# Optimization experiments

Measured on AMD Instinct MI355X. Metric: run time of the kernel, lower is better.

The kernel has to match this reference:

```python
import jax, jax.numpy as jnp
from jax import lax
import numpy as np

N = 256          # HiPPO order
DT = 1.0 / 4096  # discretization step ~ 1/L
L = 4096         # sequence length
BATCH = 64


def _legt_transition(n):
    # LegT (translated Legendre) HiPPO transition matrices (continuous-time).
    Q = np.arange(n, dtype=np.float64)
    R = (2.0 * Q + 1.0) ** 0.5
    j, i = np.meshgrid(Q, Q)
    A = R[:, None] * np.where(i < j, (-1.0) ** (i - j), 1.0) * R[None, :]
    B = R[:, None]
    return -A, B


def _bilinear_discretize(A, B, dt):
    # scipy.signal.cont2discrete(..., method='bilinear')
    n = A.shape[0]
    I = np.eye(n)
    M = np.linalg.inv(I - (dt / 2.0) * A)
    Ad = M @ (I + (dt / 2.0) * A)
    Bd = (M @ B) * dt
    return Ad, Bd


def setup_inputs() -> dict:
    key = jax.random.key(0)
    A, B = _legt_transition(N)
    Ad, Bd = _bilinear_discretize(A, B, DT)
    inputs = jax.random.normal(key, (L, BATCH), dtype=jnp.float32)
    return {
        "inputs": inputs,
        "A": jnp.asarray(Ad, dtype=jnp.float32),          # (N, N)
        "B": jnp.asarray(Bd.squeeze(-1), dtype=jnp.float32),  # (N,)
    }


def reference(inputs, A, B):
    # inputs: (L, BATCH) -> output cs: (L, BATCH, N)
    u = inputs[..., None]  # (L, BATCH, 1)
    c0 = jnp.zeros((inputs.shape[1], A.shape[0]), dtype=inputs.dtype)  # (BATCH, N)

    def step(c, f):
        # c = F.linear(c, A) + B * f  ==  c @ A^T + B * f
        c = c @ A.T + B * f
        return c, c

    _, cs = lax.scan(step, c0, u)
    return cs
```

## Files before the change

kernel.cpp:

```cpp
#include <hip/hip_runtime.h>
#include <hip/hip_bf16.h>


#define MATF 65536

typedef __attribute__((ext_vector_type(8))) short short8;
typedef __attribute__((ext_vector_type(4))) float f32x4;

__device__ __forceinline__ unsigned short f2bf(float x) {
  union { __hip_bfloat16 h; unsigned short u; } cv;
  cv.h = __float2bfloat16(x);
  return cv.u;
}
__device__ __forceinline__ float bf2f(unsigned short u) {
  union { unsigned short u; __hip_bfloat16 h; } cv;
  cv.u = u;
  return __bfloat162float(cv.h);
}

__device__ __forceinline__ void load16_lds(const void* gsrc, void* ldst) {
  __builtin_amdgcn_global_load_lds(
      (const __attribute__((address_space(1))) unsigned int*)gsrc,
      (__attribute__((address_space(3))) unsigned int*)ldst,
      16, 0, 0);
}

__global__ __launch_bounds__(256) void gemm_nn_batch(
    const float* __restrict__ X, const float* __restrict__ Ys,
    float* __restrict__ Zs, int count)
{
  int g    = blockIdx.x >> 4;
  int tile = blockIdx.x & 15;
  if (g >= count) return;
  const float* Y = Ys + (size_t)g * MATF;
  float*       Z = Zs + (size_t)g * MATF;
  int tr = (tile >> 2) * 64;
  int tc = (tile & 3) * 64;

  __shared__ float As[64][33];
  __shared__ float Bs[32][65];
  int tid = threadIdx.x;
  int tx = tid & 15, ty = tid >> 4;
  float acc[4][4] = {};

  for (int k0 = 0; k0 < 256; k0 += 32) {
#pragma unroll
    for (int p = 0; p < 2; ++p) {
      int idx = tid + p * 256;
      int r = idx >> 3, c4 = (idx & 7) * 4;
      float4 v = *(const float4*)(X + (size_t)(tr + r) * 256 + k0 + c4);
      As[r][c4 + 0] = v.x; As[r][c4 + 1] = v.y; As[r][c4 + 2] = v.z; As[r][c4 + 3] = v.w;
    }
#pragma unroll
    for (int p = 0; p < 2; ++p) {
      int idx = tid + p * 256;
      int r = idx >> 4, c4 = (idx & 15) * 4;
      float4 v = *(const float4*)(Y + (size_t)(k0 + r) * 256 + tc + c4);
      Bs[r][c4 + 0] = v.x; Bs[r][c4 + 1] = v.y; Bs[r][c4 + 2] = v.z; Bs[r][c4 + 3] = v.w;
    }
    __syncthreads();
#pragma unroll
    for (int kk = 0; kk < 32; ++kk) {
      float a[4], b[4];
#pragma unroll
      for (int u = 0; u < 4; ++u) a[u] = As[ty * 4 + u][kk];
#pragma unroll
      for (int v = 0; v < 4; ++v) b[v] = Bs[kk][tx * 4 + v];
#pragma unroll
      for (int u = 0; u < 4; ++u)
#pragma unroll
        for (int v = 0; v < 4; ++v) acc[u][v] += a[u] * b[v];
    }
    __syncthreads();
  }
#pragma unroll
  for (int u = 0; u < 4; ++u)
#pragma unroll
    for (int v = 0; v < 4; ++v)
      Z[(size_t)(tr + ty * 4 + u) * 256 + tc + tx * 4 + v] = acc[u][v];
}

__global__ __launch_bounds__(256) void pow_first(
    const float* __restrict__ A, float* __restrict__ P)
{
  int bid = blockIdx.x, tid = threadIdx.x;
  if (bid >= 16) {
    int blk = bid - 16;
#pragma unroll
    for (int q = 0; q < 4; ++q) {
      int idx = blk * 1024 + q * 256 + tid;
      *(float4*)(P + (size_t)idx * 4) = *(const float4*)(A + (size_t)idx * 4);
    }
    return;
  }
  int tile = bid;
  int tr = (tile >> 2) * 64;
  int tc = (tile & 3) * 64;
  __shared__ float As[64][33];
  __shared__ float Bs[32][65];
  int tx = tid & 15, ty = tid >> 4;
  float acc[4][4] = {};
  for (int k0 = 0; k0 < 256; k0 += 32) {
#pragma unroll
    for (int p = 0; p < 2; ++p) {
      int idx = tid + p * 256;
      int r = idx >> 3, c4 = (idx & 7) * 4;
      float4 v = *(const float4*)(A + (size_t)(tr + r) * 256 + k0 + c4);
      As[r][c4 + 0] = v.x; As[r][c4 + 1] = v.y; As[r][c4 + 2] = v.z; As[r][c4 + 3] = v.w;
    }
#pragma unroll
    for (int p = 0; p < 2; ++p) {
      int idx = tid + p * 256;
      int r = idx >> 4, c4 = (idx & 15) * 4;
      float4 v = *(const float4*)(A + (size_t)(k0 + r) * 256 + tc + c4);
      Bs[r][c4 + 0] = v.x; Bs[r][c4 + 1] = v.y; Bs[r][c4 + 2] = v.z; Bs[r][c4 + 3] = v.w;
    }
    __syncthreads();
#pragma unroll
    for (int kk = 0; kk < 32; ++kk) {
      float a[4], b[4];
#pragma unroll
      for (int u = 0; u < 4; ++u) a[u] = As[ty * 4 + u][kk];
#pragma unroll
      for (int v = 0; v < 4; ++v) b[v] = Bs[kk][tx * 4 + v];
#pragma unroll
      for (int u = 0; u < 4; ++u)
#pragma unroll
        for (int v = 0; v < 4; ++v) acc[u][v] += a[u] * b[v];
    }
    __syncthreads();
  }
#pragma unroll
  for (int u = 0; u < 4; ++u)
#pragma unroll
    for (int v = 0; v < 4; ++v)
      P[(size_t)MATF + (size_t)(tr + ty * 4 + u) * 256 + tc + tx * 4 + v] = acc[u][v];
}

__global__ __launch_bounds__(256) void kv_kernel(
    const float* __restrict__ P, const float* __restrict__ Bv,
    float* __restrict__ Kv)
{
  int j = blockIdx.x;
  int n = threadIdx.x;
  __shared__ float bs[256];
  bs[n] = Bv[n];
  __syncthreads();
  if (j == 0) { Kv[n] = bs[n]; return; }
  const float* M = P + (size_t)(j - 1) * MATF;
  float acc = 0.f;
  for (int m = 0; m < 256; ++m) acc += M[(size_t)n * 256 + m] * bs[m];
  Kv[(size_t)j * 256 + n] = acc;
}

__global__ __launch_bounds__(256) void e_kernel(
    const float* __restrict__ in, const float* __restrict__ Kv,
    float* __restrict__ e)
{
  int k = blockIdx.x >> 6;
  int b = blockIdx.x & 63;
  int n = threadIdx.x;
  __shared__ float fs[64];
  if (n < 64) fs[n] = in[(size_t)(k * 64 + n) * 64 + b];
  __syncthreads();
  float acc = 0.f;
#pragma unroll
  for (int j = 0; j < 64; ++j) acc += Kv[(size_t)j * 256 + n] * fs[63 - j];
  e[((size_t)k * 256 + n) * 64 + b] = acc;
}

__global__ __launch_bounds__(256) void scan_round(
    const float* __restrict__ win, float* __restrict__ wout,
    const float* __restrict__ M, int d,
    float* __restrict__ MSdst,
    const float* __restrict__ P, const float* __restrict__ Kv,
    unsigned short* __restrict__ Gt, int gt_row0, int gt_off)
{
  __shared__ float As[64][33];
  __shared__ float Bs[32][65];
  int bid = blockIdx.x;
  int tid = threadIdx.x;

  if (bid >= gt_off) {
    int r2 = gt_row0 + (bid - gt_off);
    if (r2 >= 16384) return;
    int i = r2 >> 8, n = r2 & 255;
    unsigned short* dst = Gt + (size_t)r2 * 640;
    for (int c = tid; c < 320; c += 256) {
      float x;
      if (c < 64) x = (c <= i) ? Kv[(size_t)(i - c) * 256 + n] : 0.f;
      else        x = P[(size_t)i * MATF + (size_t)n * 256 + (c - 64)];
      unsigned short hi = f2bf(x);
      float lo = x - bf2f(hi);
      dst[c]       = hi;
      dst[320 + c] = f2bf(lo);
    }
    return;
  }
  if (bid >= 256) {
    int tile = bid - 256;
    int tr = (tile >> 2) * 64;
    int tc = (tile & 3) * 64;
    int tx = tid & 15, ty = tid >> 4;
    float acc[4][4] = {};
    for (int k0 = 0; k0 < 256; k0 += 32) {
#pragma unroll
      for (int p = 0; p < 2; ++p) {
        int idx = tid + p * 256;
        int r = idx >> 3, c4 = (idx & 7) * 4;
        float4 v = *(const float4*)(M + (size_t)(tr + r) * 256 + k0 + c4);
        As[r][c4 + 0] = v.x; As[r][c4 + 1] = v.y; As[r][c4 + 2] = v.z; As[r][c4 + 3] = v.w;
      }
#pragma unroll
      for (int p = 0; p < 2; ++p) {
        int idx = tid + p * 256;
        int r = idx >> 4, c4 = (idx & 15) * 4;
        float4 v = *(const float4*)(M + (size_t)(k0 + r) * 256 + tc + c4);
        Bs[r][c4 + 0] = v.x; Bs[r][c4 + 1] = v.y; Bs[r][c4 + 2] = v.z; Bs[r][c4 + 3] = v.w;
      }
      __syncthreads();
#pragma unroll
      for (int kk = 0; kk < 32; ++kk) {
        float a[4], b[4];
#pragma unroll
        for (int u = 0; u < 4; ++u) a[u] = As[ty * 4 + u][kk];
#pragma unroll
        for (int v = 0; v < 4; ++v) b[v] = Bs[kk][tx * 4 + v];
#pragma unroll
        for (int u = 0; u < 4; ++u)
#pragma unroll
          for (int v = 0; v < 4; ++v) acc[u][v] += a[u] * b[v];
      }
      __syncthreads();
    }
#pragma unroll
    for (int u = 0; u < 4; ++u)
#pragma unroll
      for (int v = 0; v < 4; ++v)
        MSdst[(size_t)(tr + ty * 4 + u) * 256 + tc + tx * 4 + v] = acc[u][v];
    return;
  }

  int k  = bid >> 2;
  int rt = bid & 3;
  const float* src = win  + (size_t)k * 16384;
  float*       dst = wout + (size_t)k * 16384;
  if (k < d) {
#pragma unroll
    for (int p = 0; p < 16; ++p) {
      int idx = rt * 4096 + p * 256 + tid;
      dst[idx] = src[idx];
    }
    return;
  }
  const float* v = win + (size_t)(k - d) * 16384;
  int tx = tid & 15, ty = tid >> 4;
  float acc[4][4] = {};
  for (int k0 = 0; k0 < 256; k0 += 32) {
#pragma unroll
    for (int p = 0; p < 2; ++p) {
      int idx = tid + p * 256;
      int r = idx >> 3, c4 = (idx & 7) * 4;
      float4 t4 = *(const float4*)(M + (size_t)(rt * 64 + r) * 256 + k0 + c4);
      As[r][c4 + 0] = t4.x; As[r][c4 + 1] = t4.y; As[r][c4 + 2] = t4.z; As[r][c4 + 3] = t4.w;
    }
#pragma unroll
    for (int p = 0; p < 2; ++p) {
      int idx = tid + p * 256;
      int r = idx >> 4, c4 = (idx & 15) * 4;
      float4 t4 = *(const float4*)(v + (size_t)(k0 + r) * 64 + c4);
      Bs[r][c4 + 0] = t4.x; Bs[r][c4 + 1] = t4.y; Bs[r][c4 + 2] = t4.z; Bs[r][c4 + 3] = t4.w;
    }
    __syncthreads();
#pragma unroll
    for (int kk = 0; kk < 32; ++kk) {
      float a[4], b[4];
#pragma unroll
      for (int u = 0; u < 4; ++u) a[u] = As[ty * 4 + u][kk];
#pragma unroll
      for (int v2 = 0; v2 < 4; ++v2) b[v2] = Bs[kk][tx * 4 + v2];
#pragma unroll
      for (int u = 0; u < 4; ++u)
#pragma unroll
        for (int v2 = 0; v2 < 4; ++v2) acc[u][v2] += a[u] * b[v2];
    }
    __syncthreads();
  }
#pragma unroll
  for (int u = 0; u < 4; ++u)
#pragma unroll
    for (int v2 = 0; v2 < 4; ++v2) {
      int idx = (rt * 64 + ty * 4 + u) * 64 + tx * 4 + v2;
      dst[idx] = src[idx] + acc[u][v2];
    }
}

__global__ __launch_bounds__(320) void build_ht(
    const float* __restrict__ in, const float* __restrict__ w,
    unsigned short* __restrict__ Ht)
{
  int row = blockIdx.x;
  int k = row >> 6, b = row & 63;
  int j = threadIdx.x;
  float x;
  if (j < 64) x = in[(size_t)(k * 64 + j) * 64 + b];
  else        x = (k > 0) ? w[((size_t)(k - 1) * 256 + (j - 64)) * 64 + b] : 0.f;
  unsigned short hi = f2bf(x);
  float lo = x - bf2f(hi);
  Ht[(size_t)row * 640 + j]       = hi;
  Ht[(size_t)row * 640 + 320 + j] = f2bf(lo);
}

__global__ __launch_bounds__(512) void out_gemm(
    const unsigned short* __restrict__ Ht,
    const unsigned short* __restrict__ Gt,
    float* __restrict__ out)
{
  __shared__ char smem[65536];
  char* Ab = smem;
  char* Bb = smem + 32768;

  int bid = blockIdx.x;
  int swz = (bid & 7) * 128 + (bid >> 3);
  int mt = swz >> 6;
  int nt = swz & 63;
  int mrow0 = mt * 256, nrow0 = nt * 256;

  int tid = threadIdx.x;
  int w = tid >> 6, l = tid & 63;
  int wm = w >> 2, wn = w & 3;

  auto stage = [&](const unsigned short* src, int row0, char* lds, int k0) {
#pragma unroll
    for (int it = 0; it < 4; ++it) {
      int L = it * 8192 + tid * 16;
      int row = L >> 7;
      int p = (L >> 4) & 7;
      int o = p ^ (row & 7);
      int h = o >> 2, q = o & 3;
      const void* g = src + (size_t)(row0 + row) * 640 + h * 320 + k0 + q * 8;
      void* dst = lds + (it * 8192 + w * 1024);
      load16_lds(g, dst);
    }
  };

  stage(Ht, mrow0, Ab, 0);
  stage(Gt, nrow0, Bb, 0);

  f32x4 acc[8][4] = {};
  int rAbase = wm * 128 + (l & 15);
  int rBbase = wn * 64 + (l & 15);
  int qo = l >> 4;

  for (int ks = 0; ks < 10; ++ks) {
    __syncthreads();
    short8 bh[4], bl[4];
#pragma unroll
    for (int nf = 0; nf < 4; ++nf) {
      int r = rBbase + nf * 16;
      int ph = (qo)     ^ (r & 7);
      int pl = (4 + qo) ^ (r & 7);
      bh[nf] = *(const short8*)(Bb + r * 128 + ph * 16);
      bl[nf] = *(const short8*)(Bb + r * 128 + pl * 16);
    }
#pragma unroll
    for (int mf = 0; mf < 8; ++mf) {
      int r = rAbase + mf * 16;
      int ph = (qo)     ^ (r & 7);
      int pl = (4 + qo) ^ (r & 7);
      short8 ah = *(const short8*)(Ab + r * 128 + ph * 16);
      short8 al = *(const short8*)(Ab + r * 128 + pl * 16);
#pragma unroll
      for (int nf = 0; nf < 4; ++nf) {
        acc[mf][nf] = __builtin_amdgcn_mfma_f32_16x16x32_bf16(ah, bh[nf], acc[mf][nf], 0, 0, 0);
        acc[mf][nf] = __builtin_amdgcn_mfma_f32_16x16x32_bf16(ah, bl[nf], acc[mf][nf], 0, 0, 0);
        acc[mf][nf] = __builtin_amdgcn_mfma_f32_16x16x32_bf16(al, bh[nf], acc[mf][nf], 0, 0, 0);
      }
    }
    __syncthreads();
    if (ks < 9) {
      stage(Ht, mrow0, Ab, (ks + 1) * 32);
      stage(Gt, nrow0, Bb, (ks + 1) * 32);
    }
  }

  int Mbase = mrow0 + wm * 128 + (l >> 4) * 4;
  int Nbase = nrow0 + wn * 64 + (l & 15);
#pragma unroll
  for (int mf = 0; mf < 8; ++mf)
#pragma unroll
    for (int nf = 0; nf < 4; ++nf)
#pragma unroll
      for (int r = 0; r < 4; ++r) {
        int Mrow = Mbase + mf * 16 + r;
        int Ncol = Nbase + nf * 16;
        int k = Mrow >> 6, b = Mrow & 63;
        int i = Ncol >> 8, n = Ncol & 255;
        out[((size_t)k * 4096 + (size_t)i * 64 + b) * 256 + n] = acc[mf][nf][r];
      }
}

extern "C" void kernel_launch(void* const* d_in, const int* in_sizes, int n_in,
                              void* d_out, int out_size, void* d_ws, size_t ws_size,
                              hipStream_t stream)
{
  const float* in = (const float*)d_in[0];
  const float* A  = (const float*)d_in[1];
  const float* Bv = (const float*)d_in[2];
  float* out = (float*)d_out;
  float* ws  = (float*)d_ws;

  float* P  = ws;
  float* Kv = P  + (size_t)64 * MATF;
  float* e  = Kv + (size_t)64 * 256;
  float* w2 = e  + (size_t)64 * 16384;
  float* MS = w2 + (size_t)64 * 16384;
  unsigned short* Ht = (unsigned short*)(MS + (size_t)2 * MATF);
  unsigned short* Gt = Ht + (size_t)4096 * 640;

  pow_first<<<dim3(32), dim3(256), 0, stream>>>(A, P);
  for (int m = 2; m <= 32; m <<= 1) {
    gemm_nn_batch<<<dim3(m * 16), dim3(256), 0, stream>>>(
        P + (size_t)(m - 1) * MATF, P, P + (size_t)m * MATF, m);
  }
  kv_kernel<<<dim3(64), dim3(256), 0, stream>>>(P, Bv, Kv);
  e_kernel<<<dim3(4096), dim3(256), 0, stream>>>(in, Kv, e);

  float* bufs[2] = {e, w2};
  for (int r = 0; r < 6; ++r) {
    const float* M = (r == 0) ? (P + (size_t)63 * MATF)
                              : (MS + (size_t)((r - 1) & 1) * MATF);
    float* MSdst = MS + (size_t)(r & 1) * MATF;
    int gt_row0 = r * 2731;
    int gt_cnt  = (r < 5) ? 2731 : (16384 - 5 * 2731);
    int gt_off  = (r < 5) ? 272 : 256;
    int grid    = gt_off + gt_cnt;
    scan_round<<<dim3(grid), dim3(256), 0, stream>>>(
        bufs[r & 1], bufs[(r + 1) & 1], M, 1 << r,
        MSdst, P, Kv, Gt, gt_row0, gt_off);
  }

  build_ht<<<dim3(4096), dim3(320), 0, stream>>>(in, e, Ht);

  out_gemm<<<dim3(1024), dim3(512), 0, stream>>>(Ht, Gt, out);
}
```

Measured before the change: 384.8 us.

## Double-buffer out_gemm LDS staging with split hi/lo substages and prefetch

The out_gemm main loop now splits each K-step into hi and lo substages. Each substage fills half of a 64KB LDS double buffer, and the next substage is prefetched before the current one computes. Explicit vmcnt waits replace the two __syncthreads, and s_setprio is raised around the MFMA blocks. The LDS swizzle is redone for 64-byte rows. Global loads should now overlap with MFMA work, at the cost of more register pressure from holding ah[8] across substages, plus hand-tuned waitcnt logic that could be fragile.

```diff
diff --git a/kernel.cpp b/kernel.cpp
--- a/kernel.cpp
+++ b/kernel.cpp
@@ -317,8 +317,6 @@
     float* __restrict__ out)
 {
   __shared__ char smem[65536];
-  char* Ab = smem;
-  char* Bb = smem + 32768;
 
   int bid = blockIdx.x;
   int swz = (bid & 7) * 128 + (bid >> 3);
@@ -330,58 +328,87 @@
   int w = tid >> 6, l = tid & 63;
   int wm = w >> 2, wn = w & 3;
 
-  auto stage = [&](const unsigned short* src, int row0, char* lds, int k0) {
-#pragma unroll
-    for (int it = 0; it < 4; ++it) {
-      int L = it * 8192 + tid * 16;
-      int row = L >> 7;
-      int p = (L >> 4) & 7;
-      int o = p ^ (row & 7);
-      int h = o >> 2, q = o & 3;
-      const void* g = src + (size_t)(row0 + row) * 640 + h * 320 + k0 + q * 8;
-      void* dst = lds + (it * 8192 + w * 1024);
-      load16_lds(g, dst);
+  auto stage_ss = [&](int ss) {
+    int h = ss & 1, ks = ss >> 1;
+    char* buf = smem + (ss & 1) * 32768;
+#pragma unroll
+    for (int op = 0; op < 2; ++op) {
+      const unsigned short* src = op ? Gt : Ht;
+      int row0 = op ? nrow0 : mrow0;
+      char* lds = buf + op * 16384;
+#pragma unroll
+      for (int it = 0; it < 2; ++it) {
+        int L = it * 8192 + tid * 16;
+        int row = L >> 6;
+        int p = (L >> 4) & 3;
+        int o = p ^ ((row ^ (row >> 2)) & 3);
+        const void* g = src + (size_t)(row0 + row) * 640 + h * 320 + ks * 32 + o * 8;
+        void* dst = lds + (it * 8192 + w * 1024);
+        load16_lds(g, dst);
+      }
     }
   };
 
-  stage(Ht, mrow0, Ab, 0);
-  stage(Gt, nrow0, Bb, 0);
+  stage_ss(0);
 
   f32x4 acc[8][4] = {};
-  int rAbase = wm * 128 + (l & 15);
-  int rBbase = wn * 64 + (l & 15);
+  short8 ah[8], bh[4];
+  int rA = wm * 128 + (l & 15);
+  int rB = wn * 64 + (l & 15);
   int qo = l >> 4;
 
-  for (int ks = 0; ks < 10; ++ks) {
-    __syncthreads();
-    short8 bh[4], bl[4];
-#pragma unroll
-    for (int nf = 0; nf < 4; ++nf) {
-      int r = rBbase + nf * 16;
-      int ph = (qo)     ^ (r & 7);
-      int pl = (4 + qo) ^ (r & 7);
-      bh[nf] = *(const short8*)(Bb + r * 128 + ph * 16);
-      bl[nf] = *(const short8*)(Bb + r * 128 + pl * 16);
-    }
-#pragma unroll
-    for (int mf = 0; mf < 8; ++mf) {
-      int r = rAbase + mf * 16;
-      int ph = (qo)     ^ (r & 7);
-      int pl = (4 + qo) ^ (r & 7);
-      short8 ah = *(const short8*)(Ab + r * 128 + ph * 16);
-      short8 al = *(const short8*)(Ab + r * 128 + pl * 16);
+#pragma unroll
+  for (int ss = 0; ss < 20; ++ss) {
+    if (ss < 19) {
+      stage_ss(ss + 1);
+      asm volatile("s_waitcnt vmcnt(4)" ::: "memory");
+    } else {
+      asm volatile("s_waitcnt vmcnt(0)" ::: "memory");
+    }
+    __builtin_amdgcn_s_barrier();
+    __builtin_amdgcn_sched_barrier(0);
+    char* Ab = smem + (ss & 1) * 32768;
+    char* Bb = Ab + 16384;
+    if ((ss & 1) == 0) {
 #pragma unroll
       for (int nf = 0; nf < 4; ++nf) {
-        acc[mf][nf] = __builtin_amdgcn_mfma_f32_16x16x32_bf16(ah, bh[nf], acc[mf][nf], 0, 0, 0);
-        acc[mf][nf] = __builtin_amdgcn_mfma_f32_16x16x32_bf16(ah, bl[nf], acc[mf][nf], 0, 0, 0);
-        acc[mf][nf] = __builtin_amdgcn_mfma_f32_16x16x32_bf16(al, bh[nf], acc[mf][nf], 0, 0, 0);
-      }
-    }
-    __syncthreads();
-    if (ks < 9) {
-      stage(Ht, mrow0, Ab, (ks + 1) * 32);
-      stage(Gt, nrow0, Bb, (ks + 1) * 32);
-    }
+        int r = rB + nf * 16;
+        bh[nf] = *(const short8*)(Bb + r * 64 + (qo ^ ((r ^ (r >> 2)) & 3)) * 16);
+      }
+#pragma unroll
+      for (int mf = 0; mf < 8; ++mf) {
+        int r = rA + mf * 16;
+        ah[mf] = *(const short8*)(Ab + r * 64 + (qo ^ ((r ^ (r >> 2)) & 3)) * 16);
+      }
+      __builtin_amdgcn_s_setprio(1);
+#pragma unroll
+      for (int mf = 0; mf < 8; ++mf)
+#pragma unroll
+        for (int nf = 0; nf < 4; ++nf)
+          acc[mf][nf] = __builtin_amdgcn_mfma_f32_16x16x32_bf16(ah[mf], bh[nf], acc[mf][nf], 0, 0, 0);
+      __builtin_amdgcn_s_setprio(0);
+    } else {
+      short8 bl[4];
+#pragma unroll
+      for (int nf = 0; nf < 4; ++nf) {
+        int r = rB + nf * 16;
+        bl[nf] = *(const short8*)(Bb + r * 64 + (qo ^ ((r ^ (r >> 2)) & 3)) * 16);
+      }
+      __builtin_amdgcn_s_setprio(1);
+#pragma unroll
+      for (int mf = 0; mf < 8; ++mf) {
+        int r = rA + mf * 16;
+        short8 al = *(const short8*)(Ab + r * 64 + (qo ^ ((r ^ (r >> 2)) & 3)) * 16);
+#pragma unroll
+        for (int nf = 0; nf < 4; ++nf) {
+          acc[mf][nf] = __builtin_amdgcn_mfma_f32_16x16x32_bf16(ah[mf], bl[nf], acc[mf][nf], 0, 0, 0);
+          acc[mf][nf] = __builtin_amdgcn_mfma_f32_16x16x32_bf16(al, bh[nf], acc[mf][nf], 0, 0, 0);
+        }
+      }
+      __builtin_amdgcn_s_setprio(0);
+    }
+    __builtin_amdgcn_sched_barrier(0);
+    __builtin_amdgcn_s_barrier();
   }
 
   int Mbase = mrow0 + wm * 128 + (l >> 4) * 4;
```

New measurement: 390.2 us. About the same (+1.4%).

## Restructure chunk scan into two-level blocked scan with tiny rounds and fused apply

Applied to the files above, without the earlier changes.

Replaces the six-round full Hillis-Steele scan over 64 chunk states with three rounds inside groups of 8, a small three-round scan over the 8 group carries, and one apply kernel that adds the carries using precomputed powers A^(64q). The apply kernel also writes the bf16 hi/lo H operand directly, replacing build_ht, and the Gt/Ht packing is spread across the scan launches. This cuts the amount of full-size scan GEMM work and removes one pass over the state buffer. In exchange it adds more small launches and extra matrix-power GEMMs.

```diff
diff --git a/kernel.cpp b/kernel.cpp
--- a/kernel.cpp
+++ b/kernel.cpp
@@ -6,6 +6,13 @@
 
 typedef __attribute__((ext_vector_type(8))) short short8;
 typedef __attribute__((ext_vector_type(4))) float f32x4;
+
+struct Sq4 {
+  const float* X[4];
+  const float* Y[4];
+  float* Z[4];
+  int n;
+};
 
 __device__ __forceinline__ unsigned short f2bf(float x) {
   union { __hip_bfloat16 h; unsigned short u; } cv;
@@ -25,47 +32,40 @@
       16, 0, 0);
 }
 
-__global__ __launch_bounds__(256) void gemm_nn_batch(
-    const float* __restrict__ X, const float* __restrict__ Ys,
-    float* __restrict__ Zs, int count)
-{
-  int g    = blockIdx.x >> 4;
-  int tile = blockIdx.x & 15;
-  if (g >= count) return;
-  const float* Y = Ys + (size_t)g * MATF;
-  float*       Z = Zs + (size_t)g * MATF;
+__device__ void tile_gemm64(const float* __restrict__ X,
+                            const float* __restrict__ Y,
+                            float* __restrict__ Z, int tile,
+                            float* As, float* Bs, int tid)
+{
   int tr = (tile >> 2) * 64;
   int tc = (tile & 3) * 64;
-
-  __shared__ float As[64][33];
-  __shared__ float Bs[32][65];
-  int tid = threadIdx.x;
   int tx = tid & 15, ty = tid >> 4;
   float acc[4][4] = {};
-
   for (int k0 = 0; k0 < 256; k0 += 32) {
 #pragma unroll
     for (int p = 0; p < 2; ++p) {
       int idx = tid + p * 256;
       int r = idx >> 3, c4 = (idx & 7) * 4;
       float4 v = *(const float4*)(X + (size_t)(tr + r) * 256 + k0 + c4);
-      As[r][c4 + 0] = v.x; As[r][c4 + 1] = v.y; As[r][c4 + 2] = v.z; As[r][c4 + 3] = v.w;
+      As[r * 33 + c4 + 0] = v.x; As[r * 33 + c4 + 1] = v.y;
+      As[r * 33 + c4 + 2] = v.z; As[r * 33 + c4 + 3] = v.w;
     }
 #pragma unroll
     for (int p = 0; p < 2; ++p) {
       int idx = tid + p * 256;
       int r = idx >> 4, c4 = (idx & 15) * 4;
       float4 v = *(const float4*)(Y + (size_t)(k0 + r) * 256 + tc + c4);
-      Bs[r][c4 + 0] = v.x; Bs[r][c4 + 1] = v.y; Bs[r][c4 + 2] = v.z; Bs[r][c4 + 3] = v.w;
+      Bs[r * 65 + c4 + 0] = v.x; Bs[r * 65 + c4 + 1] = v.y;
+      Bs[r * 65 + c4 + 2] = v.z; Bs[r * 65 + c4 + 3] = v.w;
     }
     __syncthreads();
 #pragma unroll
     for (int kk = 0; kk < 32; ++kk) {
       float a[4], b[4];
 #pragma unroll
-      for (int u = 0; u < 4; ++u) a[u] = As[ty * 4 + u][kk];
-#pragma unroll
-      for (int v = 0; v < 4; ++v) b[v] = Bs[kk][tx * 4 + v];
+      for (int u = 0; u < 4; ++u) a[u] = As[(ty * 4 + u) * 33 + kk];
+#pragma unroll
+      for (int v = 0; v < 4; ++v) b[v] = Bs[kk * 65 + tx * 4 + v];
 #pragma unroll
       for (int u = 0; u < 4; ++u)
 #pragma unroll
@@ -78,6 +78,18 @@
 #pragma unroll
     for (int v = 0; v < 4; ++v)
       Z[(size_t)(tr + ty * 4 + u) * 256 + tc + tx * 4 + v] = acc[u][v];
+}
+
+__global__ __launch_bounds__(256) void gemm_nn_batch(
+    const float* __restrict__ X, const float* __restrict__ Ys,
+    float* __restrict__ Zs, int count)
+{
+  __shared__ float As[64 * 33];
+  __shared__ float Bs[32 * 65];
+  int g    = blockIdx.x >> 4;
+  if (g >= count) return;
+  tile_gemm64(X, Ys + (size_t)g * MATF, Zs + (size_t)g * MATF,
+              blockIdx.x & 15, As, Bs, threadIdx.x);
 }
 
 __global__ __launch_bounds__(256) void pow_first(
@@ -93,48 +105,9 @@
     }
     return;
   }
-  int tile = bid;
-  int tr = (tile >> 2) * 64;
-  int tc = (tile & 3) * 64;
-  __shared__ float As[64][33];
-  __shared__ float Bs[32][65];
-  int tx = tid & 15, ty = tid >> 4;
-  float acc[4][4] = {};
-  for (int k0 = 0; k0 < 256; k0 += 32) {
-#pragma unroll
-    for (int p = 0; p < 2; ++p) {
-      int idx = tid + p * 256;
-      int r = idx >> 3, c4 = (idx & 7) * 4;
-      float4 v = *(const float4*)(A + (size_t)(tr + r) * 256 + k0 + c4);
-      As[r][c4 + 0] = v.x; As[r][c4 + 1] = v.y; As[r][c4 + 2] = v.z; As[r][c4 + 3] = v.w;
-    }
-#pragma unroll
-    for (int p = 0; p < 2; ++p) {
-      int idx = tid + p * 256;
-      int r = idx >> 4, c4 = (idx & 15) * 4;
-      float4 v = *(const float4*)(A + (size_t)(k0 + r) * 256 + tc + c4);
-      Bs[r][c4 + 0] = v.x; Bs[r][c4 + 1] = v.y; Bs[r][c4 + 2] = v.z; Bs[r][c4 + 3] = v.w;
-    }
-    __syncthreads();
-#pragma unroll
-    for (int kk = 0; kk < 32; ++kk) {
-      float a[4], b[4];
-#pragma unroll
-      for (int u = 0; u < 4; ++u) a[u] = As[ty * 4 + u][kk];
-#pragma unroll
-      for (int v = 0; v < 4; ++v) b[v] = Bs[kk][tx * 4 + v];
-#pragma unroll
-      for (int u = 0; u < 4; ++u)
-#pragma unroll
-        for (int v = 0; v < 4; ++v) acc[u][v] += a[u] * b[v];
-    }
-    __syncthreads();
-  }
-#pragma unroll
-  for (int u = 0; u < 4; ++u)
-#pragma unroll
-    for (int v = 0; v < 4; ++v)
-      P[(size_t)MATF + (size_t)(tr + ty * 4 + u) * 256 + tc + tx * 4 + v] = acc[u][v];
+  __shared__ float As[64 * 33];
+  __shared__ float Bs[32 * 65];
+  tile_gemm64(A, A, P + MATF, bid, As, Bs, tid);
 }
 
 __global__ __launch_bounds__(256) void kv_kernel(
@@ -169,21 +142,21 @@
   e[((size_t)k * 256 + n) * 64 + b] = acc;
 }
 
-__global__ __launch_bounds__(256) void scan_round(
+__global__ __launch_bounds__(256) void scan_round2(
     const float* __restrict__ win, float* __restrict__ wout,
-    const float* __restrict__ M, int d,
-    float* __restrict__ MSdst,
+    const float* __restrict__ M, int d, Sq4 sq, int fc_cnt,
     const float* __restrict__ P, const float* __restrict__ Kv,
-    unsigned short* __restrict__ Gt, int gt_row0, int gt_off)
-{
-  __shared__ float As[64][33];
-  __shared__ float Bs[32][65];
-  int bid = blockIdx.x;
-  int tid = threadIdx.x;
-
-  if (bid >= gt_off) {
-    int r2 = gt_row0 + (bid - gt_off);
-    if (r2 >= 16384) return;
+    const float* __restrict__ in, unsigned short* __restrict__ Gt,
+    unsigned short* __restrict__ Ht, int gt_row0)
+{
+  __shared__ float As[64 * 33];
+  __shared__ float Bs[32 * 65];
+  int bid = blockIdx.x, tid = threadIdx.x;
+  int sq_end = 256 + 16 * sq.n;
+  int fc_end = sq_end + fc_cnt;
+
+  if (bid >= fc_end) {
+    int r2 = gt_row0 + (bid - fc_end);
     int i = r2 >> 8, n = r2 & 255;
     unsigned short* dst = Gt + (size_t)r2 * 640;
     for (int c = tid; c < 320; c += 256) {
@@ -197,47 +170,23 @@
     }
     return;
   }
+  if (bid >= sq_end) {
+    int blk = bid - sq_end;
+    for (int idx = tid; idx < 1024; idx += 256) {
+      int rr = idx >> 6, j = idx & 63;
+      int row = blk * 16 + rr;
+      int k = row >> 6, b = row & 63;
+      float x = in[(size_t)(k * 64 + j) * 64 + b];
+      unsigned short hi = f2bf(x);
+      float lo = x - bf2f(hi);
+      Ht[(size_t)row * 640 + j]       = hi;
+      Ht[(size_t)row * 640 + 320 + j] = f2bf(lo);
+    }
+    return;
+  }
   if (bid >= 256) {
-    int tile = bid - 256;
-    int tr = (tile >> 2) * 64;
-    int tc = (tile & 3) * 64;
-    int tx = tid & 15, ty = tid >> 4;
-    float acc[4][4] = {};
-    for (int k0 = 0; k0 < 256; k0 += 32) {
-#pragma unroll
-      for (int p = 0; p < 2; ++p) {
-        int idx = tid + p * 256;
-        int r = idx >> 3, c4 = (idx & 7) * 4;
-        float4 v = *(const float4*)(M + (size_t)(tr + r) * 256 + k0 + c4);
-        As[r][c4 + 0] = v.x; As[r][c4 + 1] = v.y; As[r][c4 + 2] = v.z; As[r][c4 + 3] = v.w;
-      }
-#pragma unroll
-      for (int p = 0; p < 2; ++p) {
-        int idx = tid + p * 256;
-        int r = idx >> 4, c4 = (idx & 15) * 4;
-        float4 v = *(const float4*)(M + (size_t)(k0 + r) * 256 + tc + c4);
-        Bs[r][c4 + 0] = v.x; Bs[r][c4 + 1] = v.y; Bs[r][c4 + 2] = v.z; Bs[r][c4 + 3] = v.w;
-      }
-      __syncthreads();
-#pragma unroll
-      for (int kk = 0; kk < 32; ++kk) {
-        float a[4], b[4];
-#pragma unroll
-        for (int u = 0; u < 4; ++u) a[u] = As[ty * 4 + u][kk];
-#pragma unroll
-        for (int v = 0; v < 4; ++v) b[v] = Bs[kk][tx * 4 + v];
-#pragma unroll
-        for (int u = 0; u < 4; ++u)
-#pragma unroll
-          for (int v = 0; v < 4; ++v) acc[u][v] += a[u] * b[v];
-      }
-      __syncthreads();
-    }
-#pragma unroll
-    for (int u = 0; u < 4; ++u)
-#pragma unroll
-      for (int v = 0; v < 4; ++v)
-        MSdst[(size_t)(tr + ty * 4 + u) * 256 + tc + tx * 4 + v] = acc[u][v];
+    int j = (bid - 256) >> 4;
+    tile_gemm64(sq.X[j], sq.Y[j], sq.Z[j], (bid - 256) & 15, As, Bs, tid);
     return;
   }
 
@@ -245,7 +194,7 @@
   int rt = bid & 3;
   const float* src = win  + (size_t)k * 16384;
   float*       dst = wout + (size_t)k * 16384;
-  if (k < d) {
+  if ((k & 7) < d) {
 #pragma unroll
     for (int p = 0; p < 16; ++p) {
       int idx = rt * 4096 + p * 256 + tid;
@@ -262,23 +211,25 @@
       int idx = tid + p * 256;
       int r = idx >> 3, c4 = (idx & 7) * 4;
       float4 t4 = *(const float4*)(M + (size_t)(rt * 64 + r) * 256 + k0 + c4);
-      As[r][c4 + 0] = t4.x; As[r][c4 + 1] = t4.y; As[r][c4 + 2] = t4.z; As[r][c4 + 3] = t4.w;
+      As[r * 33 + c4 + 0] = t4.x; As[r * 33 + c4 + 1] = t4.y;
+      As[r * 33 + c4 + 2] = t4.z; As[r * 33 + c4 + 3] = t4.w;
     }
 #pragma unroll
     for (int p = 0; p < 2; ++p) {
       int idx = tid + p * 256;
       int r = idx >> 4, c4 = (idx & 15) * 4;
       float4 t4 = *(const float4*)(v + (size_t)(k0 + r) * 64 + c4);
-      Bs[r][c4 + 0] = t4.x; Bs[r][c4 + 1] = t4.y; Bs[r][c4 + 2] = t4.z; Bs[r][c4 + 3] = t4.w;
+      Bs[r * 65 + c4 + 0] = t4.x; Bs[r * 65 + c4 + 1] = t4.y;
+      Bs[r * 65 + c4 + 2] = t4.z; Bs[r * 65 + c4 + 3] = t4.w;
     }
     __syncthreads();
 #pragma unroll
     for (int kk = 0; kk < 32; ++kk) {
       float a[4], b[4];
 #pragma unroll
-      for (int u = 0; u < 4; ++u) a[u] = As[ty * 4 + u][kk];
-#pragma unroll
-      for (int v2 = 0; v2 < 4; ++v2) b[v2] = Bs[kk][tx * 4 + v2];
+      for (int u = 0; u < 4; ++u) a[u] = As[(ty * 4 + u) * 33 + kk];
+#pragma unroll
+      for (int v2 = 0; v2 < 4; ++v2) b[v2] = Bs[kk * 65 + tx * 4 + v2];
 #pragma unroll
       for (int u = 0; u < 4; ++u)
 #pragma unroll
@@ -295,20 +246,129 @@
     }
 }
 
-__global__ __launch_bounds__(320) void build_ht(
-    const float* __restrict__ in, const float* __restrict__ w,
-    unsigned short* __restrict__ Ht)
-{
-  int row = blockIdx.x;
-  int k = row >> 6, b = row & 63;
-  int j = threadIdx.x;
-  float x;
-  if (j < 64) x = in[(size_t)(k * 64 + j) * 64 + b];
-  else        x = (k > 0) ? w[((size_t)(k - 1) * 256 + (j - 64)) * 64 + b] : 0.f;
-  unsigned short hi = f2bf(x);
-  float lo = x - bf2f(hi);
-  Ht[(size_t)row * 640 + j]       = hi;
-  Ht[(size_t)row * 640 + 320 + j] = f2bf(lo);
+__global__ __launch_bounds__(256) void tiny_round(
+    float* __restrict__ dst, const float* __restrict__ src,
+    const float* __restrict__ M, int d, int gather, Sq4 sq)
+{
+  int bid = blockIdx.x, tid = threadIdx.x;
+  if (bid >= 128) {
+    __shared__ float As[64 * 33];
+    __shared__ float Bs[32 * 65];
+    int j = (bid - 128) >> 4;
+    tile_gemm64(sq.X[j], sq.Y[j], sq.Z[j], (bid - 128) & 15, As, Bs, tid);
+    return;
+  }
+  int g = bid >> 4, r16 = bid & 15;
+  const float* sg = src + (size_t)(gather ? (8 * g + 7) : g) * 16384;
+  float* dg = dst + (size_t)g * 16384;
+  int r = r16 * 16 + (tid >> 4);
+  int c4 = (tid & 15) * 4;
+  float4 a = *(const float4*)(sg + (size_t)r * 64 + c4);
+  if (g < d) {
+    *(float4*)(dg + (size_t)r * 64 + c4) = a;
+    return;
+  }
+  const float* sp = src + (size_t)(gather ? (8 * (g - d) + 7) : (g - d)) * 16384;
+  float acc0 = a.x, acc1 = a.y, acc2 = a.z, acc3 = a.w;
+  for (int m = 0; m < 256; ++m) {
+    float mv = M[(size_t)r * 256 + m];
+    float4 s = *(const float4*)(sp + (size_t)m * 64 + c4);
+    acc0 += mv * s.x; acc1 += mv * s.y; acc2 += mv * s.z; acc3 += mv * s.w;
+  }
+  float4 o; o.x = acc0; o.y = acc1; o.z = acc2; o.w = acc3;
+  *(float4*)(dg + (size_t)r * 64 + c4) = o;
+}
+
+__global__ __launch_bounds__(256) void apply_kernel(
+    const float* __restrict__ w2, const float* __restrict__ C,
+    const float* __restrict__ P63, const float* __restrict__ PX,
+    const float* __restrict__ Kv, const float* __restrict__ P,
+    unsigned short* __restrict__ Gt, unsigned short* __restrict__ Ht,
+    int gt_row0)
+{
+  __shared__ float As[64 * 33];
+  __shared__ float Bs[32 * 65];
+  int bid = blockIdx.x, tid = threadIdx.x;
+  if (bid >= 260) {
+    int r2 = gt_row0 + (bid - 260);
+    int i = r2 >> 8, n = r2 & 255;
+    unsigned short* dst = Gt + (size_t)r2 * 640;
+    for (int c = tid; c < 320; c += 256) {
+      float x;
+      if (c < 64) x = (c <= i) ? Kv[(size_t)(i - c) * 256 + n] : 0.f;
+      else        x = P[(size_t)i * MATF + (size_t)n * 256 + (c - 64)];
+      unsigned short hi = f2bf(x);
+      float lo = x - bf2f(hi);
+      dst[c]       = hi;
+      dst[320 + c] = f2bf(lo);
+    }
+    return;
+  }
+  if (bid >= 252) {
+    int blk = bid - 252;
+    for (int idx = tid; idx < 8 * 512; idx += 256) {
+      int row = blk * 8 + (idx >> 9);
+      int c = idx & 511;
+      int col = (c < 256) ? (64 + c) : (128 + c);
+      Ht[(size_t)row * 640 + col] = 0;
+    }
+    return;
+  }
+
+  int k = bid >> 2, rt = bid & 3;
+  const float* w2c = w2 + (size_t)k * 16384;
+  int tx = tid & 15, ty = tid >> 4;
+  float acc[4][4] = {};
+  if (k >= 8) {
+    int g = k >> 3, q = k & 7;
+    const float* Mq = (q == 0) ? P63 : (PX + (size_t)(q - 1) * MATF);
+    const float* v = C + (size_t)(g - 1) * 16384;
+    for (int k0 = 0; k0 < 256; k0 += 32) {
+#pragma unroll
+      for (int p = 0; p < 2; ++p) {
+        int idx = tid + p * 256;
+        int r = idx >> 3, c4 = (idx & 7) * 4;
+        float4 t4 = *(const float4*)(Mq + (size_t)(rt * 64 + r) * 256 + k0 + c4);
+        As[r * 33 + c4 + 0] = t4.x; As[r * 33 + c4 + 1] = t4.y;
+        As[r * 33 + c4 + 2] = t4.z; As[r * 33 + c4 + 3] = t4.w;
+      }
+#pragma unroll
+      for (int p = 0; p < 2; ++p) {
+        int idx = tid + p * 256;
+        int r = idx >> 4, c4 = (idx & 15) * 4;
+        float4 t4 = *(const float4*)(v + (size_t)(k0 + r) * 64 + c4);
+        Bs[r * 65 + c4 + 0] = t4.x; Bs[r * 65 + c4 + 1] = t4.y;
+        Bs[r * 65 + c4 + 2] = t4.z; Bs[r * 65 + c4 + 3] = t4.w;
+      }
+      __syncthreads();
+#pragma unroll
+      for (int kk = 0; kk < 32; ++kk) {
+        float a[4], b[4];
+#pragma unroll
+        for (int u = 0; u < 4; ++u) a[u] = As[(ty * 4 + u) * 33 + kk];
+#pragma unroll
+        for (int v2 = 0; v2 < 4; ++v2) b[v2] = Bs[kk * 65 + tx * 4 + v2];
+#pragma unroll
+        for (int u = 0; u < 4; ++u)
+#pragma unroll
+          for (int v2 = 0; v2 < 4; ++v2) acc[u][v2] += a[u] * b[v2];
+      }
+      __syncthreads();
+    }
+  }
+#pragma unroll
+  for (int u = 0; u < 4; ++u)
+#pragma unroll
+    for (int v2 = 0; v2 < 4; ++v2) {
+      int n = rt * 64 + ty * 4 + u;
+      int b = tx * 4 + v2;
+      float s = acc[u][v2] + w2c[(size_t)n * 64 + b];
+      unsigned short hi = f2bf(s);
+      float lo = s - bf2f(hi);
+      size_t rowoff = (size_t)((k + 1) * 64 + b) * 640;
+      Ht[rowoff + 64 + n]  = hi;
+      Ht[rowoff + 384 + n] = f2bf(lo);
+    }
 }
 
 __global__ __launch_bounds__(512) void out_gemm(
@@ -414,9 +474,12 @@
   float* Kv = P  + (size_t)64 * MATF;
   float* e  = Kv + (size_t)64 * 256;
   float* w2 = e  + (size_t)64 * 16384;
-  float* MS = w2 + (size_t)64 * 16384;
-  unsigned short* Ht = (unsigned short*)(MS + (size_t)2 * MATF);
+  float* PX = w2 + (size_t)64 * 16384;
+  float* TA = PX + (size_t)9 * MATF;
+  float* TB = TA + (size_t)8 * 16384;
+  unsigned short* Ht = (unsigned short*)(TB + (size_t)8 * 16384);
   unsigned short* Gt = Ht + (size_t)4096 * 640;
+  const float* P63 = P + (size_t)63 * MATF;
 
   pow_first<<<dim3(32), dim3(256), 0, stream>>>(A, P);
   for (int m = 2; m <= 32; m <<= 1) {
@@ -426,21 +489,41 @@
   kv_kernel<<<dim3(64), dim3(256), 0, stream>>>(P, Bv, Kv);
   e_kernel<<<dim3(4096), dim3(256), 0, stream>>>(in, Kv, e);
 
-  float* bufs[2] = {e, w2};
-  for (int r = 0; r < 6; ++r) {
-    const float* M = (r == 0) ? (P + (size_t)63 * MATF)
-                              : (MS + (size_t)((r - 1) & 1) * MATF);
-    float* MSdst = MS + (size_t)(r & 1) * MATF;
-    int gt_row0 = r * 2731;
-    int gt_cnt  = (r < 5) ? 2731 : (16384 - 5 * 2731);
-    int gt_off  = (r < 5) ? 272 : 256;
-    int grid    = gt_off + gt_cnt;
-    scan_round<<<dim3(grid), dim3(256), 0, stream>>>(
-        bufs[r & 1], bufs[(r + 1) & 1], M, 1 << r,
-        MSdst, P, Kv, Gt, gt_row0, gt_off);
-  }
-
-  build_ht<<<dim3(4096), dim3(320), 0, stream>>>(in, e, Ht);
+  Sq4 s0{}; s0.X[0] = P63; s0.Y[0] = P63; s0.Z[0] = PX; s0.n = 1;
+  scan_round2<<<dim3(256 + 16 + 4096), dim3(256), 0, stream>>>(
+      e, w2, P63, 1, s0, 0, P, Kv, in, Gt, Ht, 0);
+
+  Sq4 s1{};
+  s1.X[0] = PX;       s1.Y[0] = PX;   s1.Z[0] = PX + 2 * (size_t)MATF;
+  s1.X[1] = PX;       s1.Y[1] = P63;  s1.Z[1] = PX + 1 * (size_t)MATF;
+  s1.n = 2;
+  scan_round2<<<dim3(256 + 32 + 256 + 4096), dim3(256), 0, stream>>>(
+      w2, e, PX, 2, s1, 256, P, Kv, in, Gt, Ht, 4096);
+
+  Sq4 s2{};
+  float* PX2 = PX + 2 * (size_t)MATF;
+  s2.X[0] = PX2; s2.Y[0] = PX2;                   s2.Z[0] = PX + 6 * (size_t)MATF;
+  s2.X[1] = PX2; s2.Y[1] = P63;                   s2.Z[1] = PX + 3 * (size_t)MATF;
+  s2.X[2] = PX2; s2.Y[2] = PX;                    s2.Z[2] = PX + 4 * (size_t)MATF;
+  s2.X[3] = PX2; s2.Y[3] = PX + 1 * (size_t)MATF; s2.Z[3] = PX + 5 * (size_t)MATF;
+  s2.n = 4;
+  scan_round2<<<dim3(256 + 64 + 4096), dim3(256), 0, stream>>>(
+      e, w2, PX2, 4, s2, 0, P, Kv, in, Gt, Ht, 8192);
+
+  Sq4 t1s{}; t1s.X[0] = PX + 6 * (size_t)MATF; t1s.Y[0] = t1s.X[0];
+  t1s.Z[0] = PX + 7 * (size_t)MATF; t1s.n = 1;
+  tiny_round<<<dim3(144), dim3(256), 0, stream>>>(
+      TA, w2, PX + 6 * (size_t)MATF, 1, 1, t1s);
+  Sq4 t2s{}; t2s.X[0] = PX + 7 * (size_t)MATF; t2s.Y[0] = t2s.X[0];
+  t2s.Z[0] = PX + 8 * (size_t)MATF; t2s.n = 1;
+  tiny_round<<<dim3(144), dim3(256), 0, stream>>>(
+      TB, TA, PX + 7 * (size_t)MATF, 2, 0, t2s);
+  Sq4 t3s{}; t3s.n = 0;
+  tiny_round<<<dim3(128), dim3(256), 0, stream>>>(
+      TA, TB, PX + 8 * (size_t)MATF, 4, 0, t3s);
+
+  apply_kernel<<<dim3(252 + 8 + 4096), dim3(256), 0, stream>>>(
+      w2, TA, P63, PX, Kv, P, Gt, Ht, 12288);
 
   out_gemm<<<dim3(1024), dim3(512), 0, stream>>>(Ht, Gt, out);
 }
```

Result: slower. 536.4 us (+39.4%).
